# Optimization experiments

Hardware: AMD Instinct MI355X
Metric: run time of the kernel (lower is better)

The kernel has to match this reference:

```python
import jax, jax.numpy as jnp
import numpy as np

N, D = 250000, 512
K = 10            # number_of_neighbours
NUM_CLASSES = 100


def _l2_norm(x):
    # row-wise L2 normalization, matching torch l2_norm (sum over dim 1, +1e-12)
    normp = jnp.sum(x * x, axis=1, keepdims=True) + 1e-12
    return x / jnp.sqrt(normp)


def setup_inputs() -> dict:
    key = jax.random.key(0)
    k1, k2, k3 = jax.random.split(key, 3)
    return {
        "embedding": jax.random.normal(k1, (D,), dtype=jnp.float32),
        "collection": jax.random.normal(k2, (N, D), dtype=jnp.float32),
        "labels_int": jax.random.randint(k3, (N,), 0, NUM_CLASSES, dtype=jnp.int64),
    }


def reference(embedding, collection, labels_int):
    coll_n = _l2_norm(collection)                    # [N, D]
    q = _l2_norm(embedding[None, :])[0]              # [D]
    cos_sim = coll_n @ q                             # [N] cosine similarity matvec
    vals, idx = jax.lax.top_k(cos_sim, 1 + K)        # top-(K+1)
    # NOTE: original source slices [1:K] (K-1 neighbors); replicated faithfully.
    neigh_idx = idx[1:K]                             # [K-1]
    probs = vals[1:K]                                # [K-1]
    preds = labels_int[neigh_idx]                    # [K-1] neighbor labels
    counts = jnp.zeros(NUM_CLASSES, jnp.int32).at[preds].add(1)
    pred_int = jnp.argmax(counts)                    # majority vote (smallest label on tie, like np.unique+argmax)
    conf_pos = jnp.argmax(preds == pred_int)         # first neighbor with the winning label
    confidence = probs[conf_pos]
    return vals, pred_int, confidence
```

## Files before the change

### kernel.cpp

```cpp
#include <hip/hip_runtime.h>

#define NROWS  250000
#define DIM    512
#define TOPK   11
#define KNEIGH 9
#define NCLS   100
#define NB     1024
#define TPB    256
#define WPB    4
#define NWAVES (NB * WPB)
#define RPW    ((NROWS + NWAVES - 1) / NWAVES)
#define NC     (NB * TOPK)

__device__ __forceinline__ bool better(float v1, int i1, float v2, int i2) {
    return (v1 > v2) || ((v1 == v2) && (i1 < i2));
}

__global__ __launch_bounds__(TPB) void knn_stage1(
    const float* __restrict__ emb,
    const float* __restrict__ coll,
    float* __restrict__ cand_v,
    int*   __restrict__ cand_i)
{
    const int lane = threadIdx.x & 63;
    const int warp = threadIdx.x >> 6;
    const int wid  = blockIdx.x * WPB + warp;

    const float4 e0 = *(const float4*)(emb + lane * 8);
    const float4 e1 = *(const float4*)(emb + lane * 8 + 4);
    float es = e0.x*e0.x + e0.y*e0.y + e0.z*e0.z + e0.w*e0.w
             + e1.x*e1.x + e1.y*e1.y + e1.z*e1.z + e1.w*e1.w;
    #pragma unroll
    for (int s = 1; s < 64; s <<= 1) es += __shfl_xor(es, s, 64);
    const float edenom = sqrtf(es + 1e-12f);

    float tv[TOPK];
    int   ti[TOPK];
    #pragma unroll
    for (int j = 0; j < TOPK; ++j) { tv[j] = -__builtin_inff(); ti[j] = 0x7fffffff; }

    const int row0 = wid * RPW;
    for (int r = 0; r < RPW; ++r) {
        const int row = row0 + r;
        if (row >= NROWS) break;
        const float* p = coll + (size_t)row * DIM + lane * 8;
        const float4 c0 = *(const float4*)p;
        const float4 c1 = *(const float4*)(p + 4);
        float dot = c0.x*e0.x + c0.y*e0.y + c0.z*e0.z + c0.w*e0.w
                  + c1.x*e1.x + c1.y*e1.y + c1.z*e1.z + c1.w*e1.w;
        float nrm = c0.x*c0.x + c0.y*c0.y + c0.z*c0.z + c0.w*c0.w
                  + c1.x*c1.x + c1.y*c1.y + c1.z*c1.z + c1.w*c1.w;
        #pragma unroll
        for (int s = 1; s < 64; s <<= 1) {
            dot += __shfl_xor(dot, s, 64);
            nrm += __shfl_xor(nrm, s, 64);
        }
        const float sim = dot / (sqrtf(nrm + 1e-12f) * edenom);
        if (better(sim, row, tv[TOPK-1], ti[TOPK-1])) {
            tv[TOPK-1] = sim; ti[TOPK-1] = row;
            #pragma unroll
            for (int j = TOPK-1; j > 0; --j) {
                if (better(tv[j], ti[j], tv[j-1], ti[j-1])) {
                    float fv = tv[j]; tv[j] = tv[j-1]; tv[j-1] = fv;
                    int   fi = ti[j]; ti[j] = ti[j-1]; ti[j-1] = fi;
                } else break;
            }
        }
    }

    __shared__ float sv[WPB * TOPK];
    __shared__ int   si[WPB * TOPK];
    if (lane == 0) {
        #pragma unroll
        for (int j = 0; j < TOPK; ++j) { sv[warp*TOPK + j] = tv[j]; si[warp*TOPK + j] = ti[j]; }
    }
    __syncthreads();
    if (warp == 0) {
        float v = (lane < WPB*TOPK) ? sv[lane] : -__builtin_inff();
        int   i = (lane < WPB*TOPK) ? si[lane] : 0x7fffffff;
        for (int r = 0; r < TOPK; ++r) {
            float bv = v; int bi = i;
            #pragma unroll
            for (int s = 1; s < 64; s <<= 1) {
                float ov = __shfl_xor(bv, s, 64);
                int   oi = __shfl_xor(bi, s, 64);
                if (better(ov, oi, bv, bi)) { bv = ov; bi = oi; }
            }
            if (v == bv && i == bi) v = -__builtin_inff();
            if (lane == 0) { cand_v[blockIdx.x*TOPK + r] = bv; cand_i[blockIdx.x*TOPK + r] = bi; }
        }
    }
}

__global__ __launch_bounds__(TPB) void knn_stage2(
    const float* __restrict__ cand_v,
    const int*   __restrict__ cand_i,
    const int*   __restrict__ labels,
    float* __restrict__ out)
{
    const int tid  = threadIdx.x;
    const int lane = tid & 63;
    const int warp = tid >> 6;

    float tv[TOPK + 1];
    int   ti[TOPK + 1];
    #pragma unroll
    for (int j = 0; j < TOPK + 1; ++j) { tv[j] = -__builtin_inff(); ti[j] = 0x7fffffff; }

    for (int j = tid; j < NC; j += TPB) {
        float v = cand_v[j]; int i = cand_i[j];
        if (better(v, i, tv[TOPK-1], ti[TOPK-1])) {
            tv[TOPK-1] = v; ti[TOPK-1] = i;
            #pragma unroll
            for (int q = TOPK-1; q > 0; --q) {
                if (better(tv[q], ti[q], tv[q-1], ti[q-1])) {
                    float fv = tv[q]; tv[q] = tv[q-1]; tv[q-1] = fv;
                    int   fi = ti[q]; ti[q] = ti[q-1]; ti[q-1] = fi;
                } else break;
            }
        }
    }

    __shared__ float lv[TPB * (TOPK + 1)];
    __shared__ int   li[TPB * (TOPK + 1)];
    #pragma unroll
    for (int j = 0; j < TOPK + 1; ++j) {
        lv[tid*(TOPK+1) + j] = tv[j];
        li[tid*(TOPK+1) + j] = ti[j];
    }

    __shared__ float rv[TOPK];
    __shared__ int   ri[TOPK];
    __shared__ float wv_[TPB/64];
    __shared__ int   wi_[TPB/64], wt_[TPB/64];
    __shared__ int   winner;
    __syncthreads();

    int p = 0;
    for (int r = 0; r < TOPK; ++r) {
        float cv = lv[tid*(TOPK+1) + p];
        int   ci = li[tid*(TOPK+1) + p];
        int   ct = tid;
        #pragma unroll
        for (int s = 1; s < 64; s <<= 1) {
            float ov = __shfl_xor(cv, s, 64);
            int   oi = __shfl_xor(ci, s, 64);
            int   ot = __shfl_xor(ct, s, 64);
            if (better(ov, oi, cv, ci)) { cv = ov; ci = oi; ct = ot; }
        }
        if (lane == 0) { wv_[warp] = cv; wi_[warp] = ci; wt_[warp] = ct; }
        __syncthreads();
        if (tid == 0) {
            float bv = wv_[0]; int bi = wi_[0]; int bt = wt_[0];
            for (int w = 1; w < TPB/64; ++w)
                if (better(wv_[w], wi_[w], bv, bi)) { bv = wv_[w]; bi = wi_[w]; bt = wt_[w]; }
            rv[r] = bv; ri[r] = bi; winner = bt;
        }
        __syncthreads();
        if (tid == winner) ++p;
    }
    __syncthreads();

    if (tid == 0) {
        #pragma unroll
        for (int j = 0; j < TOPK; ++j) out[j] = rv[j];

        int cnt[NCLS];
        for (int c = 0; c < NCLS; ++c) cnt[c] = 0;
        int preds[KNEIGH];
        for (int j = 0; j < KNEIGH; ++j) {
            preds[j] = labels[ri[1 + j]];
            ++cnt[preds[j]];
        }
        int best = 0, bc = cnt[0];
        for (int c = 1; c < NCLS; ++c) if (cnt[c] > bc) { bc = cnt[c]; best = c; }
        int cp = 0;
        for (int j = KNEIGH - 1; j >= 0; --j) if (preds[j] == best) cp = j;
        out[11] = (float)best;
        out[12] = rv[1 + cp];
    }
}

extern "C" void kernel_launch(void* const* d_in, const int* in_sizes, int n_in,
                              void* d_out, int out_size, void* d_ws, size_t ws_size,
                              hipStream_t stream) {
    const float* emb    = (const float*)d_in[0];
    const float* coll   = (const float*)d_in[1];
    const int*   labels = (const int*)d_in[2];
    float*       out    = (float*)d_out;

    float* cand_v = (float*)d_ws;
    int*   cand_i = (int*)(cand_v + NC);

    knn_stage1<<<NB, TPB, 0, stream>>>(emb, coll, cand_v, cand_i);
    knn_stage2<<<1, TPB, 0, stream>>>(cand_v, cand_i, labels, out);
}
```

Measured before the change: 731.9 us.

## Process four rows per wavefront with 16-lane groups and nontemporal loads

Each wavefront now handles four rows at once: a 16-lane group takes one row with eight float4 loads per lane, which raises the number of loads in flight. Shuffle reductions shrink from six steps to four, and rows are strided across waves instead of given out as contiguous chunks. Collection loads use nontemporal hints so the streamed data does not pollute the cache. In exchange, the top-k insertion for the four rows runs serially after a broadcast shuffle, and the query vector takes more registers.

```diff
diff --git a/kernel.cpp b/kernel.cpp
--- a/kernel.cpp
+++ b/kernel.cpp
@@ -9,8 +9,10 @@
 #define TPB    256
 #define WPB    4
 #define NWAVES (NB * WPB)
-#define RPW    ((NROWS + NWAVES - 1) / NWAVES)
+#define NGROUPS (NROWS / 4)
 #define NC     (NB * TOPK)
+
+typedef float v4f __attribute__((ext_vector_type(4)));
 
 __device__ __forceinline__ bool better(float v1, int i1, float v2, int i2) {
     return (v1 > v2) || ((v1 == v2) && (i1 < i2));
@@ -25,45 +27,62 @@
     const int lane = threadIdx.x & 63;
     const int warp = threadIdx.x >> 6;
     const int wid  = blockIdx.x * WPB + warp;
-
-    const float4 e0 = *(const float4*)(emb + lane * 8);
-    const float4 e1 = *(const float4*)(emb + lane * 8 + 4);
-    float es = e0.x*e0.x + e0.y*e0.y + e0.z*e0.z + e0.w*e0.w
-             + e1.x*e1.x + e1.y*e1.y + e1.z*e1.z + e1.w*e1.w;
-    #pragma unroll
-    for (int s = 1; s < 64; s <<= 1) es += __shfl_xor(es, s, 64);
+    const int q    = lane >> 4;
+    const int j    = lane & 15;
+
+    const float* ep = emb + 4 * j;
+    v4f e[8];
+    #pragma unroll
+    for (int c = 0; c < 8; ++c) e[c] = *(const v4f*)(ep + 64 * c);
+    float es = 0.f;
+    #pragma unroll
+    for (int c = 0; c < 8; ++c)
+        es += e[c].x*e[c].x + e[c].y*e[c].y + e[c].z*e[c].z + e[c].w*e[c].w;
+    #pragma unroll
+    for (int s = 1; s < 16; s <<= 1) es += __shfl_xor(es, s, 64);
     const float edenom = sqrtf(es + 1e-12f);
 
     float tv[TOPK];
     int   ti[TOPK];
     #pragma unroll
-    for (int j = 0; j < TOPK; ++j) { tv[j] = -__builtin_inff(); ti[j] = 0x7fffffff; }
-
-    const int row0 = wid * RPW;
-    for (int r = 0; r < RPW; ++r) {
-        const int row = row0 + r;
-        if (row >= NROWS) break;
-        const float* p = coll + (size_t)row * DIM + lane * 8;
-        const float4 c0 = *(const float4*)p;
-        const float4 c1 = *(const float4*)(p + 4);
-        float dot = c0.x*e0.x + c0.y*e0.y + c0.z*e0.z + c0.w*e0.w
-                  + c1.x*e1.x + c1.y*e1.y + c1.z*e1.z + c1.w*e1.w;
-        float nrm = c0.x*c0.x + c0.y*c0.y + c0.z*c0.z + c0.w*c0.w
-                  + c1.x*c1.x + c1.y*c1.y + c1.z*c1.z + c1.w*c1.w;
-        #pragma unroll
-        for (int s = 1; s < 64; s <<= 1) {
+    for (int t = 0; t < TOPK; ++t) { tv[t] = -__builtin_inff(); ti[t] = 0x7fffffff; }
+
+    const float* base = coll + 4 * j;
+    for (int g = wid; g < NGROUPS; g += NWAVES) {
+        const int row = 4 * g + q;
+        const float* p = base + (size_t)row * DIM;
+
+        v4f a[8];
+        #pragma unroll
+        for (int c = 0; c < 8; ++c)
+            a[c] = __builtin_nontemporal_load((const v4f*)(p + 64 * c));
+
+        float dot = 0.f, nrm = 0.f;
+        #pragma unroll
+        for (int c = 0; c < 8; ++c) {
+            dot += a[c].x*e[c].x + a[c].y*e[c].y + a[c].z*e[c].z + a[c].w*e[c].w;
+            nrm += a[c].x*a[c].x + a[c].y*a[c].y + a[c].z*a[c].z + a[c].w*a[c].w;
+        }
+        #pragma unroll
+        for (int s = 1; s < 16; s <<= 1) {
             dot += __shfl_xor(dot, s, 64);
             nrm += __shfl_xor(nrm, s, 64);
         }
-        const float sim = dot / (sqrtf(nrm + 1e-12f) * edenom);
-        if (better(sim, row, tv[TOPK-1], ti[TOPK-1])) {
-            tv[TOPK-1] = sim; ti[TOPK-1] = row;
-            #pragma unroll
-            for (int j = TOPK-1; j > 0; --j) {
-                if (better(tv[j], ti[j], tv[j-1], ti[j-1])) {
-                    float fv = tv[j]; tv[j] = tv[j-1]; tv[j-1] = fv;
-                    int   fi = ti[j]; ti[j] = ti[j-1]; ti[j-1] = fi;
-                } else break;
+        const float simq = dot / (sqrtf(nrm + 1e-12f) * edenom);
+
+        #pragma unroll
+        for (int qq = 0; qq < 4; ++qq) {
+            const float sim = __shfl(simq, qq * 16, 64);
+            const int   row_q = 4 * g + qq;
+            if (better(sim, row_q, tv[TOPK-1], ti[TOPK-1])) {
+                tv[TOPK-1] = sim; ti[TOPK-1] = row_q;
+                #pragma unroll
+                for (int t = TOPK-1; t > 0; --t) {
+                    if (better(tv[t], ti[t], tv[t-1], ti[t-1])) {
+                        float fv = tv[t]; tv[t] = tv[t-1]; tv[t-1] = fv;
+                        int   fi = ti[t]; ti[t] = ti[t-1]; ti[t-1] = fi;
+                    } else break;
+                }
             }
         }
     }
@@ -72,7 +91,7 @@
     __shared__ int   si[WPB * TOPK];
     if (lane == 0) {
         #pragma unroll
-        for (int j = 0; j < TOPK; ++j) { sv[warp*TOPK + j] = tv[j]; si[warp*TOPK + j] = ti[j]; }
+        for (int t = 0; t < TOPK; ++t) { sv[warp*TOPK + t] = tv[t]; si[warp*TOPK + t] = ti[t]; }
     }
     __syncthreads();
     if (warp == 0) {
@@ -105,17 +124,17 @@
     float tv[TOPK + 1];
     int   ti[TOPK + 1];
     #pragma unroll
-    for (int j = 0; j < TOPK + 1; ++j) { tv[j] = -__builtin_inff(); ti[j] = 0x7fffffff; }
-
-    for (int j = tid; j < NC; j += TPB) {
-        float v = cand_v[j]; int i = cand_i[j];
+    for (int t = 0; t < TOPK + 1; ++t) { tv[t] = -__builtin_inff(); ti[t] = 0x7fffffff; }
+
+    for (int c = tid; c < NC; c += TPB) {
+        float v = cand_v[c]; int i = cand_i[c];
         if (better(v, i, tv[TOPK-1], ti[TOPK-1])) {
             tv[TOPK-1] = v; ti[TOPK-1] = i;
             #pragma unroll
-            for (int q = TOPK-1; q > 0; --q) {
-                if (better(tv[q], ti[q], tv[q-1], ti[q-1])) {
-                    float fv = tv[q]; tv[q] = tv[q-1]; tv[q-1] = fv;
-                    int   fi = ti[q]; ti[q] = ti[q-1]; ti[q-1] = fi;
+            for (int t = TOPK-1; t > 0; --t) {
+                if (better(tv[t], ti[t], tv[t-1], ti[t-1])) {
+                    float fv = tv[t]; tv[t] = tv[t-1]; tv[t-1] = fv;
+                    int   fi = ti[t]; ti[t] = ti[t-1]; ti[t-1] = fi;
                 } else break;
             }
         }
@@ -124,9 +143,9 @@
     __shared__ float lv[TPB * (TOPK + 1)];
     __shared__ int   li[TPB * (TOPK + 1)];
     #pragma unroll
-    for (int j = 0; j < TOPK + 1; ++j) {
-        lv[tid*(TOPK+1) + j] = tv[j];
-        li[tid*(TOPK+1) + j] = ti[j];
+    for (int t = 0; t < TOPK + 1; ++t) {
+        lv[tid*(TOPK+1) + t] = tv[t];
+        li[tid*(TOPK+1) + t] = ti[t];
     }
 
     __shared__ float rv[TOPK];
@@ -163,19 +182,19 @@
 
     if (tid == 0) {
         #pragma unroll
-        for (int j = 0; j < TOPK; ++j) out[j] = rv[j];
+        for (int t = 0; t < TOPK; ++t) out[t] = rv[t];
 
         int cnt[NCLS];
         for (int c = 0; c < NCLS; ++c) cnt[c] = 0;
         int preds[KNEIGH];
-        for (int j = 0; j < KNEIGH; ++j) {
-            preds[j] = labels[ri[1 + j]];
-            ++cnt[preds[j]];
+        for (int t = 0; t < KNEIGH; ++t) {
+            preds[t] = labels[ri[1 + t]];
+            ++cnt[preds[t]];
         }
         int best = 0, bc = cnt[0];
         for (int c = 1; c < NCLS; ++c) if (cnt[c] > bc) { bc = cnt[c]; best = c; }
         int cp = 0;
-        for (int j = KNEIGH - 1; j >= 0; --j) if (preds[j] == best) cp = j;
+        for (int t = KNEIGH - 1; t >= 0; --t) if (preds[t] == best) cp = t;
         out[11] = (float)best;
         out[12] = rv[1 + cp];
     }
```

New measurement: 686.5 us. -6.2%, faster.
